# Kernel optimization log

Measured on AMD Instinct MI355X. Metric: run time of the kernel, lower is better.

Reference implementation:

```python
import jax, jax.numpy as jnp
import numpy as np

B, T, D, H = 4, 2048, 1024, 16
HD = D // H  # head_dim = 64


def setup_inputs() -> dict:
    key = jax.random.key(0)
    k1, k2, k3 = jax.random.split(key, 3)
    x = jax.random.normal(k1, (B, T, D), dtype=jnp.float32)
    # rotary cache: (T, head_dim/2, 2) holding (cos, sin)
    inv_freq = 1.0 / (10000.0 ** (jnp.arange(0, HD, 2, dtype=jnp.float32) / HD))  # (HD/2,)
    t = jnp.arange(T, dtype=jnp.float32)
    freqs = jnp.einsum('t,f->tf', t, inv_freq)  # (T, HD/2)
    rope = jnp.stack([jnp.cos(freqs), jnp.sin(freqs)], axis=-1)  # (T, HD/2, 2)
    # causal boolean attn mask, broadcastable (1,1,T,T)
    mask = jnp.tril(jnp.ones((T, T), dtype=bool))[None, None]
    # params (bias-free linears), scaled like nn.Linear default init
    W_attn = jax.random.normal(k2, (3 * D, D), dtype=jnp.float32) / np.sqrt(D)
    W_proj = jax.random.normal(k3, (D, D), dtype=jnp.float32) / np.sqrt(D)
    return {"x": x, "rope": rope, "mask": mask, "W_attn": W_attn, "W_proj": W_proj}


def apply_rope(x, rope):
    # x: (B, T, H, HD); rope: (T, HD/2, 2)
    b, t, h, hd = x.shape
    xr = x.reshape(b, t, h, hd // 2, 2)
    x1, x2 = xr[..., 0], xr[..., 1]
    cos = rope[None, :, None, :, 0]  # (1, T, 1, HD/2)
    sin = rope[None, :, None, :, 1]
    out = jnp.stack([x1 * cos - x2 * sin, x1 * sin + x2 * cos], axis=-1)
    return out.reshape(b, t, h, hd)


def reference(x, rope, mask, W_attn, W_proj):
    b, t, d = x.shape
    qkv = jnp.einsum('btd,ed->bte', x, W_attn)  # (B, T, 3D)
    q, k, v = jnp.split(qkv, 3, axis=2)
    q = apply_rope(q.reshape(b, t, H, HD), rope)
    k = apply_rope(k.reshape(b, t, H, HD), rope)
    v = v.reshape(b, t, H, HD)
    # (B, H, T, HD)
    q = q.transpose(0, 2, 1, 3)
    k = k.transpose(0, 2, 1, 3)
    v = v.transpose(0, 2, 1, 3)
    scale = 1.0 / np.sqrt(HD)
    scores = jnp.einsum('bhqd,bhkd->bhqk', q, k) * scale
    scores = jnp.where(mask, scores, jnp.finfo(scores.dtype).min)
    attn = jax.nn.softmax(scores, axis=-1)
    o = jnp.einsum('bhqk,bhkd->bhqd', attn, v)
    o = o.transpose(0, 2, 1, 3).reshape(b, t, d)
    return jnp.einsum('btd,ed->bte', o, W_proj)
```

## Files before the change

### kernel.cpp

```cpp
#include <hip/hip_runtime.h>

typedef unsigned short u16;
typedef unsigned int u32;
typedef unsigned long long u64;
typedef __bf16 v8bf __attribute__((ext_vector_type(8)));
typedef __bf16 v4bf __attribute__((ext_vector_type(4)));
typedef float v4f __attribute__((ext_vector_type(4)));
typedef float v16f __attribute__((ext_vector_type(16)));
typedef u32 v4u __attribute__((ext_vector_type(4)));

#define BB 4
#define TT 2048
#define HH 16
#define DD 1024

__device__ __forceinline__ u16 f2bf(float f){
  u32 u = __float_as_uint(f);
  u32 r = u + 0x7FFFu + ((u >> 16) & 1u);
  return (u16)(r >> 16);
}
__device__ __forceinline__ float bf2f(u16 h){ return __uint_as_float(((u32)h) << 16); }
__device__ __forceinline__ v16f z16(){
  v16f z;
#pragma unroll
  for (int i = 0; i < 16; i++) z[i] = 0.f;
  return z;
}
__device__ __forceinline__ u32 cvtpk(float lo, float hi){
  u32 d;
  asm("v_cvt_pk_bf16_f32 %0, %1, %2" : "=v"(d) : "v"(lo), "v"(hi));
  return d;
}
__device__ __forceinline__ void swap32(u32 &a, u32 &b){
  asm volatile("v_permlane32_swap_b32 %0, %1" : "+v"(a), "+v"(b));
}

typedef __attribute__((address_space(1))) const void gas_t;
typedef __attribute__((address_space(3))) void las_t;
__device__ __forceinline__ void gl_lds16(const void* g, void* l){
  __builtin_amdgcn_global_load_lds((gas_t*)g, (las_t*)l, 16, 0, 0);
}

__global__ __launch_bounds__(256) void k_convert(
    const float* __restrict__ x, const float* __restrict__ wa,
    const float* __restrict__ wp, u16* __restrict__ xb,
    u16* __restrict__ wab, u16* __restrict__ wpb){
  int i = blockIdx.x * 256 + threadIdx.x;
  const int nxq = (BB*TT*DD) / 4;
  const int naq = (3*DD*DD) / 4;
  const float* src; u16* dst; int j;
  if (i < nxq)            { src = x;  dst = xb;  j = i; }
  else if (i < nxq + naq) { src = wa; dst = wab; j = i - nxq; }
  else                    { src = wp; dst = wpb; j = i - nxq - naq; }
  float4 v = reinterpret_cast<const float4*>(src)[j];
  u64 p = (u64)f2bf(v.x) | ((u64)f2bf(v.y) << 16)
        | ((u64)f2bf(v.z) << 32) | ((u64)f2bf(v.w) << 48);
  reinterpret_cast<u64*>(dst)[j] = p;
}

__global__ __launch_bounds__(256) void k_gemm_bt(
    const u16* __restrict__ A, const u16* __restrict__ Bt,
    const float* __restrict__ rope,
    int M, int N, int K, int mode, float* __restrict__ Cf,
    u16* __restrict__ qo, u16* __restrict__ ko, u16* __restrict__ vo){
  __shared__ char smem[32768];
  char* As = smem;
  char* Bs = smem + 16384;
  const int t = threadIdx.x;
  const int lane = t & 63, w = t >> 6;
  const int c = lane & 15, g = lane >> 4;
  const int nbn = N >> 7;
  const int chunk = gridDim.x >> 3;
  const int swzb = (blockIdx.x & 7) * chunk + (blockIdx.x >> 3);
  const int bm = swzb / nbn, bn = swzb % nbn;
  const long arow0 = (long)bm * 128;
  const long brow0 = (long)bn * 128;
  const int wrow = (w >> 1) * 64, wcol = (w & 1) * 64;

  v4f acc[4][4];
#pragma unroll
  for (int i = 0; i < 4; i++)
#pragma unroll
    for (int j = 0; j < 4; j++){ v4f z = {0.f,0.f,0.f,0.f}; acc[i][j] = z; }

  for (int k0 = 0; k0 < K; k0 += 64){
    __syncthreads();
#pragma unroll
    for (int i = 0; i < 4; i++){
      int slot = t + i * 256;
      int row  = slot >> 3;
      int cb   = (slot & 7) << 4;
      int scb  = cb ^ ((row & 7) << 4);
      gl_lds16((const char*)A  + ((arow0 + row) * (long)K + k0) * 2 + scb,
               As + ((t & 192) + i * 256) * 16);
      gl_lds16((const char*)Bt + ((brow0 + row) * (long)K + k0) * 2 + scb,
               Bs + ((t & 192) + i * 256) * 16);
    }
    __syncthreads();

    v8bf af[4][2], bfr[4][2];
#pragma unroll
    for (int mt = 0; mt < 4; mt++){
      int row = wrow + mt * 16 + c;
      int sw  = (row & 7) << 4;
#pragma unroll
      for (int ks = 0; ks < 2; ks++)
        af[mt][ks] = *(const v8bf*)(As + row * 128 + ((ks * 64 + g * 16) ^ sw));
    }
#pragma unroll
    for (int nt = 0; nt < 4; nt++){
      int row = wcol + nt * 16 + c;
      int sw  = (row & 7) << 4;
#pragma unroll
      for (int ks = 0; ks < 2; ks++)
        bfr[nt][ks] = *(const v8bf*)(Bs + row * 128 + ((ks * 64 + g * 16) ^ sw));
    }
#pragma unroll
    for (int mt = 0; mt < 4; mt++)
#pragma unroll
      for (int nt = 0; nt < 4; nt++)
#pragma unroll
        for (int ks = 0; ks < 2; ks++)
          acc[mt][nt] = __builtin_amdgcn_mfma_f32_16x16x32_bf16(
              af[mt][ks], bfr[nt][ks], acc[mt][nt], 0, 0, 0);
  }

  if (mode == 1){
#pragma unroll
    for (int mt = 0; mt < 4; mt++)
#pragma unroll
      for (int nt = 0; nt < 4; nt++)
#pragma unroll
        for (int r = 0; r < 4; r++){
          long row = arow0 + wrow + mt * 16 + g * 4 + r;
          long col = brow0 + wcol + nt * 16 + c;
          Cf[row * N + col] = acc[mt][nt][r];
        }
  } else {
    const int t0 = (int)(arow0 & 2047);
    __syncthreads();
#pragma unroll
    for (int l = 0; l < 8; l++)
      gl_lds16((const char*)rope + (size_t)t0 * 256 + (size_t)(t + l * 256) * 16,
               smem + ((t & 192) + l * 256) * 16);
    __syncthreads();

    const long bb = arow0 >> 11;
#pragma unroll
    for (int mt = 0; mt < 4; mt++){
      const int tposb = wrow + mt * 16 + g * 4;
#pragma unroll
      for (int nt = 0; nt < 4; nt++){
        int e    = (int)brow0 + wcol + nt * 16 + c;
        int tsel = e >> 10;
        int hh   = (e >> 6) & 15;
        int d    = e & 63;
        if (tsel == 2){
          v4bf pk;
#pragma unroll
          for (int r = 0; r < 4; r++) pk[r] = (__bf16)acc[mt][nt][r];
          *(v4bf*)(vo + (((bb * HH + hh) * 64 + d) << 11) + t0 + tposb) = pk;
        } else {
          const float qs = tsel ? 1.0f : 0.18033688011112042f;
          const int f = d >> 1;
          const bool odd = d & 1;
          u16* dst = tsel ? ko : qo;
          long base = ((bb * HH + hh) * TT + t0 + tposb) * 64 + d;
#pragma unroll
          for (int r = 0; r < 4; r++){
            float v = acc[mt][nt][r];
            float2 cn = *(const float2*)(smem + (tposb + r) * 256 + f * 8);
            float px = __shfl_xor(v, 1, 64);
            float o = odd ? (px * cn.y + v * cn.x) : (v * cn.x - px * cn.y);
            dst[base + (long)r * 64] = f2bf(o * qs);
          }
        }
      }
    }
  }
}

__global__ __launch_bounds__(256) void k_attn(
    const u16* __restrict__ Q, const u16* __restrict__ K,
    const u16* __restrict__ Vt, u16* __restrict__ O){
  __shared__ char smem[16384];
  char* ksm = smem;
  char* vsm = smem + 8192;
  int bx = blockIdx.x;
  int bh = bx & 63;
  int bt = 15 - (bx >> 6);
  int q0 = bt * 128;
  int b = bh >> 4, h = bh & 15;
  const u16* Qb = Q  + (size_t)bh * TT * 64;
  const u16* Kb = K  + (size_t)bh * TT * 64;
  const u16* Vb = Vt + (size_t)bh * 64 * TT;
  const int t = threadIdx.x, lane = t & 63, w = t >> 6;
  const int c = lane & 31, hi = lane >> 5;
  const int swz = (c & 7) << 4;
  const int wq0 = q0 + w * 32;

  v8bf qf[4];
  {
    const u16* qrow = Qb + (size_t)(wq0 + c) * 64 + hi * 8;
#pragma unroll
    for (int kc = 0; kc < 4; kc++) qf[kc] = *(const v8bf*)(qrow + kc * 16);
  }

  float m_ = -1e30f, l_ = 0.f;
  v16f accO0 = z16(), accO1 = z16();

  for (int kv0 = 0; kv0 < q0 + 128; kv0 += 64){
    __syncthreads();
#pragma unroll
    for (int i = 0; i < 2; i++){
      int s   = t + i * 256;
      int row = s >> 3;
      int cb  = (s & 7) << 4;
      int scb = cb ^ ((row & 7) << 4);
      gl_lds16((const char*)Kb + (size_t)(kv0 + row) * 128 + scb,
               ksm + ((t & 192) + i * 256) * 16);
      gl_lds16((const char*)Vb + (size_t)row * (TT * 2) + (size_t)kv0 * 2 + scb,
               vsm + ((t & 192) + i * 256) * 16);
    }
    __syncthreads();

    if (kv0 <= wq0 + 31){
      v16f s0 = z16(), s1 = z16();
      __builtin_amdgcn_s_setprio(1);
#pragma unroll
      for (int kc = 0; kc < 4; kc++){
        int off = (kc * 32 + hi * 16) ^ swz;
        v8bf a0 = *(const v8bf*)(ksm + c * 128 + off);
        v8bf a1 = *(const v8bf*)(ksm + (32 + c) * 128 + off);
        s0 = __builtin_amdgcn_mfma_f32_32x32x16_bf16(a0, qf[kc], s0, 0, 0, 0);
        s1 = __builtin_amdgcn_mfma_f32_32x32x16_bf16(a1, qf[kc], s1, 0, 0, 0);
      }
      __builtin_amdgcn_s_setprio(0);
      if (kv0 + 63 > wq0){
        int q = wq0 + c;
#pragma unroll
        for (int r = 0; r < 16; r++){
          int crow = (r & 3) + 8 * (r >> 2) + 4 * hi;
          if (kv0 + crow > q)      s0[r] = -1e30f;
          if (kv0 + 32 + crow > q) s1[r] = -1e30f;
        }
      }
      float mx = -1e30f;
#pragma unroll
      for (int r = 0; r < 16; r++){ mx = fmaxf(mx, s0[r]); mx = fmaxf(mx, s1[r]); }
      mx = fmaxf(mx, __shfl_xor(mx, 32, 64));
      if (!__all(mx - m_ <= 8.0f)){
        float mn = fmaxf(m_, mx);
        float alpha = __builtin_amdgcn_exp2f(m_ - mn);
        m_ = mn;
        l_ *= alpha;
#pragma unroll
        for (int r = 0; r < 16; r++){ accO0[r] *= alpha; accO1[r] *= alpha; }
      }
      float sum = 0.f;
#pragma unroll
      for (int r = 0; r < 16; r++){
        float p0 = __builtin_amdgcn_exp2f(s0[r] - m_);
        float p1 = __builtin_amdgcn_exp2f(s1[r] - m_);
        s0[r] = p0; s1[r] = p1;
        sum += p0 + p1;
      }
      sum += __shfl_xor(sum, 32, 64);
      l_ += sum;
      v8bf pbf[4];
      {
        u32 wd[16];
#pragma unroll
        for (int i = 0; i < 8; i++) wd[i]     = cvtpk(s0[2*i], s0[2*i+1]);
#pragma unroll
        for (int i = 0; i < 8; i++) wd[8 + i] = cvtpk(s1[2*i], s1[2*i+1]);
        swap32(wd[0], wd[2]);  swap32(wd[1], wd[3]);
        swap32(wd[4], wd[6]);  swap32(wd[5], wd[7]);
        swap32(wd[8], wd[10]); swap32(wd[9], wd[11]);
        swap32(wd[12], wd[14]); swap32(wd[13], wd[15]);
        v4u u0 = {wd[0], wd[1], wd[2], wd[3]};
        v4u u1 = {wd[4], wd[5], wd[6], wd[7]};
        v4u u2 = {wd[8], wd[9], wd[10], wd[11]};
        v4u u3 = {wd[12], wd[13], wd[14], wd[15]};
        pbf[0] = __builtin_bit_cast(v8bf, u0);
        pbf[1] = __builtin_bit_cast(v8bf, u1);
        pbf[2] = __builtin_bit_cast(v8bf, u2);
        pbf[3] = __builtin_bit_cast(v8bf, u3);
      }
      __builtin_amdgcn_s_setprio(1);
#pragma unroll
      for (int kc = 0; kc < 4; kc++){
        int off = (kc * 32 + hi * 16) ^ swz;
        v8bf va0 = *(const v8bf*)(vsm + c * 128 + off);
        v8bf va1 = *(const v8bf*)(vsm + (32 + c) * 128 + off);
        accO0 = __builtin_amdgcn_mfma_f32_32x32x16_bf16(va0, pbf[kc], accO0, 0, 0, 0);
        accO1 = __builtin_amdgcn_mfma_f32_32x32x16_bf16(va1, pbf[kc], accO1, 0, 0, 0);
      }
      __builtin_amdgcn_s_setprio(0);
    }
  }

  float inv = __builtin_amdgcn_rcpf(l_);
  int q = wq0 + c;
  u16* orow = O + ((size_t)(b * TT + q)) * DD + h * 64;
#pragma unroll
  for (int q4 = 0; q4 < 4; q4++){
    v4bf o0, o1;
#pragma unroll
    for (int j = 0; j < 4; j++){
      o0[j] = (__bf16)(accO0[q4 * 4 + j] * inv);
      o1[j] = (__bf16)(accO1[q4 * 4 + j] * inv);
    }
    *(v4bf*)(orow + q4 * 8 + hi * 4)      = o0;
    *(v4bf*)(orow + 32 + q4 * 8 + hi * 4) = o1;
  }
}

extern "C" void kernel_launch(void* const* d_in, const int* in_sizes, int n_in,
                              void* d_out, int out_size, void* d_ws, size_t ws_size,
                              hipStream_t stream){
  const float* x    = (const float*)d_in[0];
  const float* rope = (const float*)d_in[1];
  const float* Wa   = (const float*)d_in[3];
  const float* Wp   = (const float*)d_in[4];

  char* ws = (char*)d_ws;
  u16* xb  = (u16*)(ws);
  u16* wab = (u16*)(ws + (16u << 20));
  u16* wpb = (u16*)(ws + (22u << 20));
  u16* qb  = (u16*)(ws + (24u << 20));
  u16* kb  = (u16*)(ws + (40u << 20));
  u16* vtb = (u16*)(ws + (56u << 20));
  u16* ob  = xb;

  k_convert<<<dim3(12288), dim3(256), 0, stream>>>(x, Wa, Wp, xb, wab, wpb);
  k_gemm_bt<<<dim3(24 * 64), dim3(256), 0, stream>>>(
      xb, wab, rope, 8192, 3072, 1024, 0, nullptr, qb, kb, vtb);
  k_attn<<<dim3(1024), dim3(256), 0, stream>>>(qb, kb, vtb, ob);
  k_gemm_bt<<<dim3(8 * 64), dim3(256), 0, stream>>>(
      ob, wpb, nullptr, 8192, 1024, 1024, 1, (float*)d_out,
      nullptr, nullptr, nullptr);
}
```

Before: 166.2 us.

## Load K and V fragments directly from global memory, dropping LDS staging

The attention kernel stops staging K and V tiles in shared memory with block-wide barriers. Each wave now reads its MFMA operands straight from global memory (relying on L1/L2 caching) and runs its own causal loop bound, with no __syncthreads. Launch bounds now request 4 blocks per CU. This removes the barriers and the LDS copy, but the four waves of a block now fetch the same K/V data separately, and uncoalesced per-lane global loads can add latency.

```diff
diff --git a/kernel.cpp b/kernel.cpp
--- a/kernel.cpp
+++ b/kernel.cpp
@@ -180,24 +180,23 @@
   }
 }
 
-__global__ __launch_bounds__(256) void k_attn(
+__global__ __launch_bounds__(256, 4) void k_attn(
     const u16* __restrict__ Q, const u16* __restrict__ K,
     const u16* __restrict__ Vt, u16* __restrict__ O){
-  __shared__ char smem[16384];
-  char* ksm = smem;
-  char* vsm = smem + 8192;
   int bx = blockIdx.x;
   int bh = bx & 63;
   int bt = 15 - (bx >> 6);
   int q0 = bt * 128;
   int b = bh >> 4, h = bh & 15;
-  const u16* Qb = Q  + (size_t)bh * TT * 64;
-  const u16* Kb = K  + (size_t)bh * TT * 64;
-  const u16* Vb = Vt + (size_t)bh * 64 * TT;
+  const u16* Qb = Q + (size_t)bh * TT * 64;
   const int t = threadIdx.x, lane = t & 63, w = t >> 6;
   const int c = lane & 31, hi = lane >> 5;
-  const int swz = (c & 7) << 4;
   const int wq0 = q0 + w * 32;
+
+  const char* kp0 = (const char*)(K  + (size_t)bh * TT * 64) + (size_t)c * 128 + hi * 16;
+  const char* kp1 = kp0 + 32 * 128;
+  const char* vp0 = (const char*)(Vt + (size_t)bh * 64 * TT) + (size_t)c * (TT * 2) + hi * 16;
+  const char* vp1 = vp0 + 32 * (TT * 2);
 
   v8bf qf[4];
   {
@@ -209,95 +208,79 @@
   float m_ = -1e30f, l_ = 0.f;
   v16f accO0 = z16(), accO1 = z16();
 
-  for (int kv0 = 0; kv0 < q0 + 128; kv0 += 64){
-    __syncthreads();
-#pragma unroll
-    for (int i = 0; i < 2; i++){
-      int s   = t + i * 256;
-      int row = s >> 3;
-      int cb  = (s & 7) << 4;
-      int scb = cb ^ ((row & 7) << 4);
-      gl_lds16((const char*)Kb + (size_t)(kv0 + row) * 128 + scb,
-               ksm + ((t & 192) + i * 256) * 16);
-      gl_lds16((const char*)Vb + (size_t)row * (TT * 2) + (size_t)kv0 * 2 + scb,
-               vsm + ((t & 192) + i * 256) * 16);
-    }
-    __syncthreads();
-
-    if (kv0 <= wq0 + 31){
-      v16f s0 = z16(), s1 = z16();
-      __builtin_amdgcn_s_setprio(1);
-#pragma unroll
-      for (int kc = 0; kc < 4; kc++){
-        int off = (kc * 32 + hi * 16) ^ swz;
-        v8bf a0 = *(const v8bf*)(ksm + c * 128 + off);
-        v8bf a1 = *(const v8bf*)(ksm + (32 + c) * 128 + off);
-        s0 = __builtin_amdgcn_mfma_f32_32x32x16_bf16(a0, qf[kc], s0, 0, 0, 0);
-        s1 = __builtin_amdgcn_mfma_f32_32x32x16_bf16(a1, qf[kc], s1, 0, 0, 0);
+  for (int kv0 = 0; kv0 < wq0 + 32; kv0 += 64){
+    v16f s0 = z16(), s1 = z16();
+    __builtin_amdgcn_s_setprio(1);
+#pragma unroll
+    for (int kc = 0; kc < 4; kc++){
+      v8bf a0 = *(const v8bf*)(kp0 + kc * 32);
+      v8bf a1 = *(const v8bf*)(kp1 + kc * 32);
+      s0 = __builtin_amdgcn_mfma_f32_32x32x16_bf16(a0, qf[kc], s0, 0, 0, 0);
+      s1 = __builtin_amdgcn_mfma_f32_32x32x16_bf16(a1, qf[kc], s1, 0, 0, 0);
+    }
+    __builtin_amdgcn_s_setprio(0);
+    if (kv0 + 63 > wq0){
+      int q = wq0 + c;
+#pragma unroll
+      for (int r = 0; r < 16; r++){
+        int crow = (r & 3) + 8 * (r >> 2) + 4 * hi;
+        if (kv0 + crow > q)      s0[r] = -1e30f;
+        if (kv0 + 32 + crow > q) s1[r] = -1e30f;
       }
-      __builtin_amdgcn_s_setprio(0);
-      if (kv0 + 63 > wq0){
-        int q = wq0 + c;
-#pragma unroll
-        for (int r = 0; r < 16; r++){
-          int crow = (r & 3) + 8 * (r >> 2) + 4 * hi;
-          if (kv0 + crow > q)      s0[r] = -1e30f;
-          if (kv0 + 32 + crow > q) s1[r] = -1e30f;
-        }
-      }
-      float mx = -1e30f;
-#pragma unroll
-      for (int r = 0; r < 16; r++){ mx = fmaxf(mx, s0[r]); mx = fmaxf(mx, s1[r]); }
-      mx = fmaxf(mx, __shfl_xor(mx, 32, 64));
-      if (!__all(mx - m_ <= 8.0f)){
-        float mn = fmaxf(m_, mx);
-        float alpha = __builtin_amdgcn_exp2f(m_ - mn);
-        m_ = mn;
-        l_ *= alpha;
-#pragma unroll
-        for (int r = 0; r < 16; r++){ accO0[r] *= alpha; accO1[r] *= alpha; }
-      }
-      float sum = 0.f;
-#pragma unroll
-      for (int r = 0; r < 16; r++){
-        float p0 = __builtin_amdgcn_exp2f(s0[r] - m_);
-        float p1 = __builtin_amdgcn_exp2f(s1[r] - m_);
-        s0[r] = p0; s1[r] = p1;
-        sum += p0 + p1;
-      }
-      sum += __shfl_xor(sum, 32, 64);
-      l_ += sum;
-      v8bf pbf[4];
-      {
-        u32 wd[16];
-#pragma unroll
-        for (int i = 0; i < 8; i++) wd[i]     = cvtpk(s0[2*i], s0[2*i+1]);
-#pragma unroll
-        for (int i = 0; i < 8; i++) wd[8 + i] = cvtpk(s1[2*i], s1[2*i+1]);
-        swap32(wd[0], wd[2]);  swap32(wd[1], wd[3]);
-        swap32(wd[4], wd[6]);  swap32(wd[5], wd[7]);
-        swap32(wd[8], wd[10]); swap32(wd[9], wd[11]);
-        swap32(wd[12], wd[14]); swap32(wd[13], wd[15]);
-        v4u u0 = {wd[0], wd[1], wd[2], wd[3]};
-        v4u u1 = {wd[4], wd[5], wd[6], wd[7]};
-        v4u u2 = {wd[8], wd[9], wd[10], wd[11]};
-        v4u u3 = {wd[12], wd[13], wd[14], wd[15]};
-        pbf[0] = __builtin_bit_cast(v8bf, u0);
-        pbf[1] = __builtin_bit_cast(v8bf, u1);
-        pbf[2] = __builtin_bit_cast(v8bf, u2);
-        pbf[3] = __builtin_bit_cast(v8bf, u3);
-      }
-      __builtin_amdgcn_s_setprio(1);
-#pragma unroll
-      for (int kc = 0; kc < 4; kc++){
-        int off = (kc * 32 + hi * 16) ^ swz;
-        v8bf va0 = *(const v8bf*)(vsm + c * 128 + off);
-        v8bf va1 = *(const v8bf*)(vsm + (32 + c) * 128 + off);
-        accO0 = __builtin_amdgcn_mfma_f32_32x32x16_bf16(va0, pbf[kc], accO0, 0, 0, 0);
-        accO1 = __builtin_amdgcn_mfma_f32_32x32x16_bf16(va1, pbf[kc], accO1, 0, 0, 0);
-      }
-      __builtin_amdgcn_s_setprio(0);
-    }
+    }
+    float mx = -1e30f;
+#pragma unroll
+    for (int r = 0; r < 16; r++){ mx = fmaxf(mx, s0[r]); mx = fmaxf(mx, s1[r]); }
+    mx = fmaxf(mx, __shfl_xor(mx, 32, 64));
+    if (!__all(mx - m_ <= 8.0f)){
+      float mn = fmaxf(m_, mx);
+      float alpha = __builtin_amdgcn_exp2f(m_ - mn);
+      m_ = mn;
+      l_ *= alpha;
+#pragma unroll
+      for (int r = 0; r < 16; r++){ accO0[r] *= alpha; accO1[r] *= alpha; }
+    }
+    float sum = 0.f;
+#pragma unroll
+    for (int r = 0; r < 16; r++){
+      float p0 = __builtin_amdgcn_exp2f(s0[r] - m_);
+      float p1 = __builtin_amdgcn_exp2f(s1[r] - m_);
+      s0[r] = p0; s1[r] = p1;
+      sum += p0 + p1;
+    }
+    sum += __shfl_xor(sum, 32, 64);
+    l_ += sum;
+    v8bf pbf[4];
+    {
+      u32 wd[16];
+#pragma unroll
+      for (int i = 0; i < 8; i++) wd[i]     = cvtpk(s0[2*i], s0[2*i+1]);
+#pragma unroll
+      for (int i = 0; i < 8; i++) wd[8 + i] = cvtpk(s1[2*i], s1[2*i+1]);
+      swap32(wd[0], wd[2]);  swap32(wd[1], wd[3]);
+      swap32(wd[4], wd[6]);  swap32(wd[5], wd[7]);
+      swap32(wd[8], wd[10]); swap32(wd[9], wd[11]);
+      swap32(wd[12], wd[14]); swap32(wd[13], wd[15]);
+      v4u u0 = {wd[0], wd[1], wd[2], wd[3]};
+      v4u u1 = {wd[4], wd[5], wd[6], wd[7]};
+      v4u u2 = {wd[8], wd[9], wd[10], wd[11]};
+      v4u u3 = {wd[12], wd[13], wd[14], wd[15]};
+      pbf[0] = __builtin_bit_cast(v8bf, u0);
+      pbf[1] = __builtin_bit_cast(v8bf, u1);
+      pbf[2] = __builtin_bit_cast(v8bf, u2);
+      pbf[3] = __builtin_bit_cast(v8bf, u3);
+    }
+    __builtin_amdgcn_s_setprio(1);
+#pragma unroll
+    for (int kc = 0; kc < 4; kc++){
+      v8bf va0 = *(const v8bf*)(vp0 + kc * 32);
+      v8bf va1 = *(const v8bf*)(vp1 + kc * 32);
+      accO0 = __builtin_amdgcn_mfma_f32_32x32x16_bf16(va0, pbf[kc], accO0, 0, 0, 0);
+      accO1 = __builtin_amdgcn_mfma_f32_32x32x16_bf16(va1, pbf[kc], accO1, 0, 0, 0);
+    }
+    __builtin_amdgcn_s_setprio(0);
+    kp0 += 64 * 128; kp1 += 64 * 128;
+    vp0 += 128;      vp1 += 128;
   }
 
   float inv = __builtin_amdgcn_rcpf(l_);
```

Measured after the change: 251.9 us. 1.52x slower.
